# Kernel tuning notes

Hardware: AMD Instinct MI355X
Metric: run time of the kernel (lower is better)

## Reference

```python
import jax, jax.numpy as jnp
import numpy as np

KH = KW = 3
STRIDE = 1
PAD = 1
K_CHUNK = 16  # chunk size along the C*kh*kw patch dim to bound the [N,F,kc,L] intermediate


def _unfold(x):
    # Mirrors torch.nn.functional.unfold: output [N, C*KH*KW, Ho*Wo], c-major then (kh, kw).
    N, C, H, W = x.shape
    Ho = (H - KH + 2 * PAD) // STRIDE + 1
    Wo = (W - KW + 2 * PAD) // STRIDE + 1
    xp = jnp.pad(x, ((0, 0), (0, 0), (PAD, PAD), (PAD, PAD)))
    pats = jnp.stack(
        [xp[:, :, i:i + STRIDE * Ho:STRIDE, j:j + STRIDE * Wo:STRIDE]
         for i in range(KH) for j in range(KW)],
        axis=2,
    )  # [N, C, KH*KW, Ho, Wo]
    return pats.reshape(N, C * KH * KW, Ho * Wo), Ho, Wo


def _chunk_dist(xc, wc):
    # xc: [N, kc, L], wc: [F, kc] -> partial L1 sums over this K-chunk: [N, F, L]
    return jnp.abs(xc[:, None, :, :] - wc[None, :, :, None]).sum(axis=2)


def _adder2d(x, W):
    # out[n, f, i, j] = -sum_k |Xcol[n, k, l] - Wcol[f, k]|  (AdderNet L1 'correlation')
    N = x.shape[0]
    F = W.shape[0]
    Xcol, Ho, Wo = _unfold(x)          # [N, K, L]
    Wcol = W.reshape(F, -1)            # [F, K]
    K = Wcol.shape[1]
    chunk = jax.checkpoint(_chunk_dist)  # remat so backward never stores [N,F,K,L] signs
    acc = jnp.zeros((N, F, Ho * Wo), x.dtype)
    for s in range(0, K, K_CHUNK):     # fixed structural loop over patch dim (K=288 -> 18 chunks)
        acc = acc + chunk(Xcol[:, s:s + K_CHUNK, :], Wcol[:, s:s + K_CHUNK])
    return -acc.reshape(N, F, Ho, Wo)


def setup_inputs() -> dict:
    key = jax.random.key(0)
    kx, kw = jax.random.split(key)
    x = jax.random.normal(kx, (16, 32, 56, 56), dtype=jnp.float32)
    # kaiming_normal_ scale on [64,32,3,3]: std = sqrt(2 / fan_in), fan_in = 32*3*3
    W = jax.random.normal(kw, (64, 32, 3, 3), dtype=jnp.float32) * np.sqrt(2.0 / (32 * 3 * 3)).astype(np.float32)
    return {"x": x, "W": W}


def reference(x, W):
    return _adder2d(x, W)
```

## Files before the change

kernel.cpp:

```cpp
#include <hip/hip_runtime.h>


#define H_   56
#define C_   32
#define F_   64
#define N_   16
#define HW_  (H_ * H_)
#define FPW  8
#define NFG  (F_ / FPW)
#define NT   49
#define WPAD_ELTS (C_ * F_ * 12)

__global__ __launch_bounds__(64)
void prep_w(const float* __restrict__ w, float* __restrict__ wpad) {
    int idx = blockIdx.x * 64 + threadIdx.x;
    if (idx >= WPAD_ELTS) return;
    int c   = idx / (F_ * 12);
    int rem = idx % (F_ * 12);
    int f   = rem / 12;
    int kk  = rem % 12;
    wpad[idx] = (kk < 9) ? w[f * (C_ * 9) + c * 9 + kk] : 0.0f;
}

__global__ __launch_bounds__(64)
void adder_main(const float* __restrict__ x,
                const float* __restrict__ wpad,
                float* __restrict__ out) {
    const int lane = threadIdx.x;
    const int lr = lane >> 3;
    const int lc = lane & 7;
    const int bid = blockIdx.x;
    const int fg = bid & (NFG - 1);
    const int t  = (bid >> 3) % NT;
    const int n  = bid / (NT * NFG);
    const int r0 = (t / 7) * 8;
    const int c0 = (t % 7) * 8;
    const int f0 = fg * FPW;

    int   off[9];
    float msk[9];
    #pragma unroll
    for (int kh = 0; kh < 3; ++kh) {
        #pragma unroll
        for (int kw = 0; kw < 3; ++kw) {
            int rp = r0 + lr + kh - 1;
            int cp = c0 + lc + kw - 1;
            bool v = (rp >= 0 && rp < H_ && cp >= 0 && cp < H_);
            off[kh * 3 + kw] = v ? rp * H_ + cp : 0;
            msk[kh * 3 + kw] = v ? 1.0f : 0.0f;
        }
    }

    float acc[FPW];
    #pragma unroll
    for (int f = 0; f < FPW; ++f) acc[f] = 0.0f;

    const float* xb = x + n * C_ * HW_;

    #pragma unroll 2
    for (int c = 0; c < C_; ++c) {
        float xv[9];
        #pragma unroll
        for (int k = 0; k < 9; ++k)
            xv[k] = xb[c * HW_ + off[k]] * msk[k];

        const float* wp = wpad + (c * F_ + f0) * 12;
        #pragma unroll
        for (int f = 0; f < FPW; ++f) {
            #pragma unroll
            for (int k = 0; k < 9; ++k)
                acc[f] += fabsf(xv[k] - wp[f * 12 + k]);
        }
    }

    const int orow = r0 + lr, ocol = c0 + lc;
    #pragma unroll
    for (int f = 0; f < FPW; ++f)
        out[((n * F_ + f0 + f) * H_ + orow) * H_ + ocol] = -acc[f];
}

extern "C" void kernel_launch(void* const* d_in, const int* in_sizes, int n_in,
                              void* d_out, int out_size, void* d_ws, size_t ws_size,
                              hipStream_t stream) {
    const float* x = (const float*)d_in[0];
    const float* w = (const float*)d_in[1];
    float* out  = (float*)d_out;
    float* wpad = (float*)d_ws;

    prep_w<<<dim3((WPAD_ELTS + 63) / 64), dim3(64), 0, stream>>>(w, wpad);
    adder_main<<<dim3(N_ * NT * NFG), dim3(64), 0, stream>>>(x, wpad, out);
}
```

Measured before the change: 94.75 us.

## Tile by output row with buffer loads and scalar weight loads

Each block now covers one full output row (56 of 64 lanes active) rather than an 8x8 tile. Input reads use raw buffer loads whose descriptor bounds return zero for padding, which removes the offset and mask arithmetic. Weights are repacked per channel and filter group so they come in through scalar buffer loads into SGPRs. The channel loop is software-pipelined with double-buffered input registers. In exchange, 8 of the 64 lanes sit idle, and correctness now depends on out-of-range buffer loads returning zero.

```diff
diff --git a/kernel.cpp b/kernel.cpp
--- a/kernel.cpp
+++ b/kernel.cpp
@@ -1,82 +1,132 @@
 #include <hip/hip_runtime.h>
+#include <stdint.h>
+#include <stddef.h>
 
 
+#define N_   16
+#define C_   32
 #define H_   56
-#define C_   32
 #define F_   64
-#define N_   16
-#define HW_  (H_ * H_)
+#define HW_  3136
 #define FPW  8
-#define NFG  (F_ / FPW)
-#define NT   49
-#define WPAD_ELTS (C_ * F_ * 12)
+#define NFG  8
+#define ROWB 224
+#define WQ_ELTS (C_ * NFG * 96)
+
+typedef int    int32x4 __attribute__((ext_vector_type(4)));
+typedef float  f32x16  __attribute__((ext_vector_type(16)));
+typedef float  f32x8   __attribute__((ext_vector_type(8)));
+
+__device__ float  __buf_load_f32(int32x4 srsrc, int voffset, int soffset, int aux) __asm("llvm.amdgcn.raw.buffer.load.f32");
+__device__ f32x16 __sbuf_load_v16(int32x4 srsrc, int soffset, int aux) __asm("llvm.amdgcn.s.buffer.load.v16f32");
+__device__ f32x8  __sbuf_load_v8 (int32x4 srsrc, int soffset, int aux) __asm("llvm.amdgcn.s.buffer.load.v8f32");
+
+__device__ inline int32x4 make_srd(const void* p, int bytes) {
+    union { const void* p; uint32_t u[2]; } a; a.p = p;
+    int32x4 r;
+    r.x = (int)a.u[0];
+    r.y = (int)a.u[1];
+    r.z = bytes;
+    r.w = 0x00020000;
+    return r;
+}
 
 __global__ __launch_bounds__(64)
-void prep_w(const float* __restrict__ w, float* __restrict__ wpad) {
+void prep_w(const float* __restrict__ w, float* __restrict__ wq) {
     int idx = blockIdx.x * 64 + threadIdx.x;
-    if (idx >= WPAD_ELTS) return;
-    int c   = idx / (F_ * 12);
-    int rem = idx % (F_ * 12);
-    int f   = rem / 12;
-    int kk  = rem % 12;
-    wpad[idx] = (kk < 9) ? w[f * (C_ * 9) + c * 9 + kk] : 0.0f;
+    if (idx >= WQ_ELTS) return;
+    int slot = idx % 96;
+    int cg   = idx / 96;
+    int c    = cg / NFG;
+    int fg   = cg % NFG;
+    int fi   = slot / 9;
+    int kk   = slot % 9;
+    float v = 0.0f;
+    if (slot < 72)
+        v = w[((fg * 8 + fi) * C_ + c) * 9 + kk];
+    wq[idx] = v;
 }
 
 __global__ __launch_bounds__(64)
 void adder_main(const float* __restrict__ x,
-                const float* __restrict__ wpad,
+                const float* __restrict__ wq,
                 float* __restrict__ out) {
     const int lane = threadIdx.x;
-    const int lr = lane >> 3;
-    const int lc = lane & 7;
-    const int bid = blockIdx.x;
-    const int fg = bid & (NFG - 1);
-    const int t  = (bid >> 3) % NT;
-    const int n  = bid / (NT * NFG);
-    const int r0 = (t / 7) * 8;
-    const int c0 = (t % 7) * 8;
-    const int f0 = fg * FPW;
+    const int bid  = blockIdx.x;
+    const int fg   = bid & (NFG - 1);
+    const int bid2 = bid >> 3;
+    const int row  = bid2 % H_;
+    const int n    = bid2 / H_;
+    const int f0   = fg * FPW;
 
-    int   off[9];
-    float msk[9];
-    #pragma unroll
-    for (int kh = 0; kh < 3; ++kh) {
-        #pragma unroll
-        for (int kw = 0; kw < 3; ++kw) {
-            int rp = r0 + lr + kh - 1;
-            int cp = c0 + lc + kw - 1;
-            bool v = (rp >= 0 && rp < H_ && cp >= 0 && cp < H_);
-            off[kh * 3 + kw] = v ? rp * H_ + cp : 0;
-            msk[kh * 3 + kw] = v ? 1.0f : 0.0f;
+    const int vA = (lane - 1) * 4;
+    const int vB = lane * 4;
+
+    const int nr0 = (row >= 1)      ? ROWB : 0;
+    const int nr2 = (row <= H_ - 2) ? ROWB : 0;
+
+    const float* xb = x + (size_t)n * C_ * HW_ + (ptrdiff_t)(row - 1) * H_;
+
+    const int32x4 wsrd = make_srd(wq, WQ_ELTS * 4);
+    const int wgbase = fg * 96 * 4;
+
+    float acc[FPW];
+#pragma unroll
+    for (int f = 0; f < FPW; ++f) acc[f] = 0.0f;
+
+    float xva[9], xvb[9];
+
+    auto load_ch = [&](int c, float* v) {
+        const float* b = xb + (size_t)c * HW_;
+        int32x4 s0 = make_srd(b,          nr0);
+        int32x4 s1 = make_srd(b + H_,     ROWB);
+        int32x4 s2 = make_srd(b + 2 * H_, nr2);
+        v[0] = __buf_load_f32(s0, vA, 0, 0);
+        v[1] = __buf_load_f32(s0, vB, 0, 0);
+        v[2] = __buf_load_f32(s0, vB, 4, 0);
+        v[3] = __buf_load_f32(s1, vA, 0, 0);
+        v[4] = __buf_load_f32(s1, vB, 0, 0);
+        v[5] = __buf_load_f32(s1, vB, 4, 0);
+        v[6] = __buf_load_f32(s2, vA, 0, 0);
+        v[7] = __buf_load_f32(s2, vB, 0, 0);
+        v[8] = __buf_load_f32(s2, vB, 4, 0);
+    };
+
+    auto compute = [&](int c, const float* cur) {
+        const int wb = c * (NFG * 96 * 4) + wgbase;
+        f32x16 w0 = __sbuf_load_v16(wsrd, wb,       0);
+        f32x16 w1 = __sbuf_load_v16(wsrd, wb + 64,  0);
+        f32x16 w2 = __sbuf_load_v16(wsrd, wb + 128, 0);
+        f32x16 w3 = __sbuf_load_v16(wsrd, wb + 192, 0);
+        f32x8  w4 = __sbuf_load_v8 (wsrd, wb + 256, 0);
+#pragma unroll
+        for (int f = 0; f < FPW; ++f) {
+#pragma unroll
+            for (int k = 0; k < 9; ++k) {
+                const int i = f * 9 + k;
+                const float wv = (i < 16) ? w0[i]
+                               : (i < 32) ? w1[i - 16]
+                               : (i < 48) ? w2[i - 32]
+                               : (i < 64) ? w3[i - 48]
+                               :            w4[i - 64];
+                acc[f] += fabsf(cur[k] - wv);
+            }
         }
+    };
+
+    load_ch(0, xva);
+    for (int c = 0; c < C_; c += 2) {
+        load_ch(c + 1, xvb);
+        compute(c, xva);
+        if (c + 2 < C_) load_ch(c + 2, xva);
+        compute(c + 1, xvb);
     }
 
-    float acc[FPW];
-    #pragma unroll
-    for (int f = 0; f < FPW; ++f) acc[f] = 0.0f;
-
-    const float* xb = x + n * C_ * HW_;
-
-    #pragma unroll 2
-    for (int c = 0; c < C_; ++c) {
-        float xv[9];
-        #pragma unroll
-        for (int k = 0; k < 9; ++k)
-            xv[k] = xb[c * HW_ + off[k]] * msk[k];
-
-        const float* wp = wpad + (c * F_ + f0) * 12;
-        #pragma unroll
-        for (int f = 0; f < FPW; ++f) {
-            #pragma unroll
-            for (int k = 0; k < 9; ++k)
-                acc[f] += fabsf(xv[k] - wp[f * 12 + k]);
-        }
+    if (lane < H_) {
+#pragma unroll
+        for (int f = 0; f < FPW; ++f)
+            out[(size_t)(n * F_ + f0 + f) * HW_ + row * H_ + lane] = -acc[f];
     }
-
-    const int orow = r0 + lr, ocol = c0 + lc;
-    #pragma unroll
-    for (int f = 0; f < FPW; ++f)
-        out[((n * F_ + f0 + f) * H_ + orow) * H_ + ocol] = -acc[f];
 }
 
 extern "C" void kernel_launch(void* const* d_in, const int* in_sizes, int n_in,
@@ -84,9 +134,9 @@
                               hipStream_t stream) {
     const float* x = (const float*)d_in[0];
     const float* w = (const float*)d_in[1];
-    float* out  = (float*)d_out;
-    float* wpad = (float*)d_ws;
+    float* out = (float*)d_out;
+    float* wqp = (float*)d_ws;
 
-    prep_w<<<dim3((WPAD_ELTS + 63) / 64), dim3(64), 0, stream>>>(w, wpad);
-    adder_main<<<dim3(N_ * NT * NFG), dim3(64), 0, stream>>>(x, wpad, out);
+    prep_w<<<dim3((WQ_ELTS + 63) / 64), dim3(64), 0, stream>>>(w, wqp);
+    adder_main<<<dim3(N_ * H_ * NFG), dim3(64), 0, stream>>>(x, wqp, out);
 }
```

Result: faster. 76.65 us (-19.1%).
